# Kernel optimization log

Hardware: AMD Instinct MI355X
Metric: run time of the kernel (lower is better)

Reference implementation:

```python
import jax, jax.numpy as jnp
import numpy as np

S = 7  # output_size
B, C, HF, WF = 8, 256, 160, 160
N = 128
IMG = 640


def setup_inputs() -> dict:
    key = jax.random.key(0)
    k1, k2, k3, k4 = jax.random.split(key, 4)
    feature_map = jax.random.normal(k1, (B, C, HF, WF), jnp.float32)
    # boxes in image-pixel coordinates (the module divides by image_size itself)
    pts = jax.random.uniform(k2, (B, N, 2, 2), jnp.float32, 0.0, float(IMG))
    lo = jnp.min(pts, axis=2)  # (x1, y1)
    hi = jnp.max(pts, axis=2)  # (x2, y2)
    bboxes = jnp.concatenate([lo, hi], axis=-1)  # [B, N, 4]
    proj_w = jax.random.normal(k3, (C, C), jnp.float32) * (1.0 / np.sqrt(C))
    proj_b = jax.random.normal(k4, (C,), jnp.float32) * 0.01
    return {"feature_map": feature_map, "bboxes": bboxes,
            "proj_w": proj_w, "proj_b": proj_b,
            "image_h": IMG, "image_w": IMG}


def _forward(feature_map, bboxes, proj_w, proj_b, image_h, image_w):
    Bb, Cc, Hf, Wf = feature_map.shape
    # 1x1 conv projection
    f = jnp.einsum('bchw,oc->bohw', feature_map, proj_w) + proj_b[None, :, None, None]
    # scale boxes from image coords to feature coords, then integer clip (as in torch code)
    sx = float(Wf) / float(image_w)
    sy = float(Hf) / float(image_h)
    x1 = jnp.clip(jnp.floor(bboxes[..., 0] * sx).astype(jnp.int32), 0, Wf - 1)
    y1 = jnp.clip(jnp.floor(bboxes[..., 1] * sy).astype(jnp.int32), 0, Hf - 1)
    x2 = jnp.clip(jnp.floor(bboxes[..., 2] * sx).astype(jnp.int32), x1 + 1, Wf)
    y2 = jnp.clip(jnp.floor(bboxes[..., 3] * sy).astype(jnp.int32), y1 + 1, Hf)
    Lx = x2 - x1  # [B, N], >= 1 by construction
    Ly = y2 - y1
    i = jnp.arange(S, dtype=jnp.int32)
    # adaptive_avg_pool2d bin edges: start=floor(i*L/S), end=ceil((i+1)*L/S)
    rs = y1[..., None] + (i * Ly[..., None]) // S            # [B, N, S]
    re = y1[..., None] + ((i + 1) * Ly[..., None] + S - 1) // S
    cs = x1[..., None] + (i * Lx[..., None]) // S
    ce = x1[..., None] + ((i + 1) * Lx[..., None] + S - 1) // S
    # summed-area table (zero-padded): I[b,c,y,x] = sum of f[b,c,:y,:x]
    I = jnp.cumsum(jnp.cumsum(f, axis=2), axis=3)
    I = jnp.pad(I, ((0, 0), (0, 0), (1, 0), (1, 0)))

    def per_batch(Ib, rs_b, re_b, cs_b, ce_b):
        # Ib: [C, Hf+1, Wf+1]; index arrays: [N, S]
        tl = Ib[:, rs_b[:, :, None], cs_b[:, None, :]]
        tr = Ib[:, rs_b[:, :, None], ce_b[:, None, :]]
        bl = Ib[:, re_b[:, :, None], cs_b[:, None, :]]
        br = Ib[:, re_b[:, :, None], ce_b[:, None, :]]
        return br - tr - bl + tl  # [C, N, S, S]

    sums = jax.vmap(per_batch)(I, rs, re, cs, ce)  # [B, C, N, S, S]
    counts = ((re - rs)[..., :, None] * (ce - cs)[..., None, :]).astype(f.dtype)  # [B, N, S, S]
    region_features = jnp.transpose(sums, (0, 2, 1, 3, 4)) / counts[:, :, None, :, :]
    # area in raw bbox units, as in the original code
    area_ratios = (bboxes[..., 2] - bboxes[..., 0]) * (bboxes[..., 3] - bboxes[..., 1])
    return region_features, area_ratios


def reference(feature_map, bboxes, proj_w, proj_b, image_h, image_w):
    return _forward(feature_map, bboxes, proj_w, proj_b, image_h, image_w)
```

## Files before the change

### kernel.cpp

```cpp
#include <hip/hip_runtime.h>
#include <hip/hip_bf16.h>

#define BB 8
#define NN 128
#define CC 256
#define HFD 160
#define WFD 160
#define SS 7
#define REGION_OUT_ELEMS (8*128*256*49)

typedef short short8 __attribute__((ext_vector_type(8)));
typedef float f32x4  __attribute__((ext_vector_type(4)));

__global__ __launch_bounds__(256) void k0_convert_w(const float* __restrict__ W,
                                                    __hip_bfloat16* __restrict__ Wb) {
    int o = blockIdx.x;
    int c = threadIdx.x;
    Wb[o * CC + c] = __float2bfloat16(W[o * CC + c]);
}

__global__ __launch_bounds__(256) void k1_rowsum_transpose(const float* __restrict__ fm,
                                                           float* __restrict__ R) {
    int bid = blockIdx.x;
    int cq  = bid & 3;
    int bh  = bid >> 2;
    int h   = bh % HFD;
    int b   = bh / HFD;
    int c0  = cq * 64;
    int t   = threadIdx.x;

    __shared__ float tile[64][161];
    __shared__ float segsum[64][5];

    #pragma unroll
    for (int it = 0; it < 10; ++it) {
        int vid = it * 256 + t;
        int c_l = vid / 40;
        int wq  = vid - c_l * 40;
        float4 v = *(const float4*)(fm + (((size_t)(b * CC + c0 + c_l)) * HFD + h) * WFD + wq * 4);
        tile[c_l][wq * 4 + 0] = v.x;
        tile[c_l][wq * 4 + 1] = v.y;
        tile[c_l][wq * 4 + 2] = v.z;
        tile[c_l][wq * 4 + 3] = v.w;
    }
    __syncthreads();

    int seg = t >> 6;
    int row = t & 63;
    {
        float s = 0.f;
        int w0 = seg * 40;
        #pragma unroll 8
        for (int k = 0; k < 40; ++k) {
            s += tile[row][w0 + k];
            tile[row][w0 + k] = s;
        }
        segsum[row][seg] = s;
    }
    __syncthreads();
    if (t < 64) {
        float a0 = segsum[t][0];
        float a1 = a0 + segsum[t][1];
        float a2 = a1 + segsum[t][2];
        segsum[t][1] = a0;
        segsum[t][2] = a1;
        segsum[t][3] = a2;
    }
    __syncthreads();
    if (seg > 0) {
        float off = segsum[row][seg];
        int w0 = seg * 40;
        #pragma unroll 8
        for (int k = 0; k < 40; ++k) tile[row][w0 + k] += off;
    }
    __syncthreads();

    size_t obase = (((size_t)b * HFD + h) * WFD) * CC + c0;
    #pragma unroll
    for (int it = 0; it < 10; ++it) {
        int vid = it * 256 + t;
        int w   = vid >> 4;
        int cg  = vid & 15;
        float4 o;
        o.x = tile[cg * 4 + 0][w];
        o.y = tile[cg * 4 + 1][w];
        o.z = tile[cg * 4 + 2][w];
        o.w = tile[cg * 4 + 3][w];
        *(float4*)(R + obase + (size_t)w * CC + cg * 4) = o;
    }
}

__global__ __launch_bounds__(64) void k2_colsum(float* __restrict__ I) {
    int w = blockIdx.x % WFD;
    int b = blockIdx.x / WFD;
    int c4 = threadIdx.x * 4;
    float* p = I + (((size_t)b * HFD) * WFD + w) * CC + c4;
    const size_t stride = (size_t)WFD * CC;
    float sx = 0.f, sy = 0.f, sz = 0.f, sw = 0.f;
    #pragma unroll 8
    for (int h = 0; h < HFD; ++h) {
        float4 v = *(float4*)(p + (size_t)h * stride);
        sx += v.x; sy += v.y; sz += v.z; sw += v.w;
        float4 s = {sx, sy, sz, sw};
        *(float4*)(p + (size_t)h * stride) = s;
    }
}

#define PB_STRIDE 264

__global__ __launch_bounds__(256) void k3_gather_gemm(
        const float* __restrict__ I, const __hip_bfloat16* __restrict__ Wb,
        const float* __restrict__ bias, const float* __restrict__ bboxes,
        const int* __restrict__ ih_p, const int* __restrict__ iw_p,
        float* __restrict__ out) {
    int bn = blockIdx.x;
    int b  = bn >> 7;
    int t  = threadIdx.x;

    __shared__ __hip_bfloat16 Pb[64 * PB_STRIDE];

    float bx1 = bboxes[bn * 4 + 0];
    float by1 = bboxes[bn * 4 + 1];
    float bx2 = bboxes[bn * 4 + 2];
    float by2 = bboxes[bn * 4 + 3];
    float sx = (float)WFD / (float)iw_p[0];
    float sy = (float)HFD / (float)ih_p[0];

    int x1 = min(max((int)floorf(bx1 * sx), 0), WFD - 1);
    int y1 = min(max((int)floorf(by1 * sy), 0), HFD - 1);
    int x2 = min(max((int)floorf(bx2 * sx), x1 + 1), WFD);
    int y2 = min(max((int)floorf(by2 * sy), y1 + 1), HFD);
    int Lx = x2 - x1, Ly = y2 - y1;

    int rs[SS], re[SS], cs[SS], ce[SS];
    #pragma unroll
    for (int i = 0; i < SS; ++i) {
        rs[i] = y1 + (i * Ly) / SS;
        re[i] = y1 + ((i + 1) * Ly + SS - 1) / SS;
        cs[i] = x1 + (i * Lx) / SS;
        ce[i] = x1 + ((i + 1) * Lx + SS - 1) / SS;
    }

    #pragma unroll
    for (int r = 49; r < 64; ++r) Pb[r * PB_STRIDE + t] = __float2bfloat16(0.f);

    {
        const int c = t;
        const size_t Ib = (size_t)b * HFD * WFD * CC;
        #pragma unroll
        for (int i = 0; i < SS; ++i) {
            int r0 = rs[i] - 1, r1 = re[i] - 1;
            float rh = (float)(re[i] - rs[i]);
            #pragma unroll
            for (int j = 0; j < SS; ++j) {
                int c0 = cs[j] - 1, c1 = ce[j] - 1;
                float br = I[Ib + ((size_t)(r1 * WFD + c1)) * CC + c];
                float tr = (r0 >= 0) ? I[Ib + ((size_t)(r0 * WFD + c1)) * CC + c] : 0.f;
                float bl = (c0 >= 0) ? I[Ib + ((size_t)(r1 * WFD + c0)) * CC + c] : 0.f;
                float tl = (r0 >= 0 && c0 >= 0) ? I[Ib + ((size_t)(r0 * WFD + c0)) * CC + c] : 0.f;
                float cnt = rh * (float)(ce[j] - cs[j]);
                Pb[(i * SS + j) * PB_STRIDE + c] = __float2bfloat16((br - tr - bl + tl) / cnt);
            }
        }
    }
    __syncthreads();

    {
        const int lane = t & 63;
        const int wv   = t >> 6;
        const int ln   = lane & 15;
        const int quad = lane >> 4;
        const int ob0  = wv * 64;

        f32x4 z = {0.f, 0.f, 0.f, 0.f};
        f32x4 acc[4][4];
        #pragma unroll
        for (int mt = 0; mt < 4; ++mt)
            #pragma unroll
            for (int nt = 0; nt < 4; ++nt) acc[mt][nt] = z;

        #pragma unroll
        for (int k0 = 0; k0 < CC; k0 += 32) {
            short8 a[4], bf[4];
            #pragma unroll
            for (int mt = 0; mt < 4; ++mt)
                a[mt] = *(const short8*)((const short*)Wb + (ob0 + mt * 16 + ln) * CC + k0 + quad * 8);
            #pragma unroll
            for (int nt = 0; nt < 4; ++nt)
                bf[nt] = *(const short8*)((const short*)Pb + (nt * 16 + ln) * PB_STRIDE + k0 + quad * 8);
            #pragma unroll
            for (int mt = 0; mt < 4; ++mt)
                #pragma unroll
                for (int nt = 0; nt < 4; ++nt)
                    acc[mt][nt] = __builtin_amdgcn_mfma_f32_16x16x32_bf16(a[mt], bf[nt], acc[mt][nt], 0, 0, 0);
        }

        size_t obase = (size_t)bn * CC * 49;
        #pragma unroll
        for (int mt = 0; mt < 4; ++mt) {
            f32x4 bv = *(const f32x4*)(bias + ob0 + mt * 16 + quad * 4);
            #pragma unroll
            for (int nt = 0; nt < 4; ++nt) {
                int cell = nt * 16 + ln;
                if (cell < 49) {
                    #pragma unroll
                    for (int reg = 0; reg < 4; ++reg) {
                        int o = ob0 + mt * 16 + quad * 4 + reg;
                        out[obase + (size_t)o * 49 + cell] = acc[mt][nt][reg] + bv[reg];
                    }
                }
            }
        }
    }

    if (t == 0) {
        out[REGION_OUT_ELEMS + bn] = (bx2 - bx1) * (by2 - by1);
    }
}

extern "C" void kernel_launch(void* const* d_in, const int* in_sizes, int n_in,
                              void* d_out, int out_size, void* d_ws, size_t ws_size,
                              hipStream_t stream) {
    const float* fm     = (const float*)d_in[0];
    const float* bboxes = (const float*)d_in[1];
    const float* W      = (const float*)d_in[2];
    const float* bias   = (const float*)d_in[3];
    const int*   ih     = (const int*)d_in[4];
    const int*   iw     = (const int*)d_in[5];
    float* out = (float*)d_out;

    __hip_bfloat16* Wb = (__hip_bfloat16*)d_ws;
    float* I = (float*)((char*)d_ws + (size_t)CC * CC * 2 + 256);
    I = (float*)(((uintptr_t)I + 1023) & ~(uintptr_t)1023);

    k0_convert_w<<<CC, 256, 0, stream>>>(W, Wb);
    k1_rowsum_transpose<<<BB * HFD * 4, 256, 0, stream>>>(fm, I);
    k2_colsum<<<BB * WFD, 64, 0, stream>>>(I);
    k3_gather_gemm<<<BB * NN, 256, 0, stream>>>(I, Wb, bias, bboxes, ih, iw, out);
}
```

Baseline: 462.0 us.

## Split gather and GEMM into separate kernels, reorder SAT column/row scans

Moves the column prefix-sum onto the original NCHW feature map as its own kernel before the row-scan/transpose. Also splits the fused gather+GEMM into a gather kernel that writes pooled bf16 cells to a workspace and a GEMM kernel that packs 64 dense cells per block, so the 15 of 64 padding columns per box are no longer wasted. This costs an extra full-size fp32 intermediate buffer (C1) and an extra round trip of pooled data through global memory.

```diff
diff --git a/kernel.cpp b/kernel.cpp
--- a/kernel.cpp
+++ b/kernel.cpp
@@ -8,6 +8,7 @@
 #define WFD 160
 #define SS 7
 #define REGION_OUT_ELEMS (8*128*256*49)
+#define NTOT (BB*NN*49)
 
 typedef short short8 __attribute__((ext_vector_type(8)));
 typedef float f32x4  __attribute__((ext_vector_type(4)));
@@ -19,8 +20,22 @@
     Wb[o * CC + c] = __float2bfloat16(W[o * CC + c]);
 }
 
-__global__ __launch_bounds__(256) void k1_rowsum_transpose(const float* __restrict__ fm,
-                                                           float* __restrict__ R) {
+__global__ __launch_bounds__(256) void k1_colsum(const float* __restrict__ fm,
+                                                 float* __restrict__ C1) {
+    int g  = blockIdx.x * 256 + threadIdx.x;
+    int bc = g / WFD;
+    int w  = g - bc * WFD;
+    size_t base = (size_t)bc * (HFD * WFD) + w;
+    float s = 0.f;
+    #pragma unroll 8
+    for (int h = 0; h < HFD; ++h) {
+        s += fm[base + (size_t)h * WFD];
+        C1[base + (size_t)h * WFD] = s;
+    }
+}
+
+__global__ __launch_bounds__(256) void k2_rowsum_transpose(const float* __restrict__ C1,
+                                                           float* __restrict__ I) {
     int bid = blockIdx.x;
     int cq  = bid & 3;
     int bh  = bid >> 2;
@@ -37,7 +52,7 @@
         int vid = it * 256 + t;
         int c_l = vid / 40;
         int wq  = vid - c_l * 40;
-        float4 v = *(const float4*)(fm + (((size_t)(b * CC + c0 + c_l)) * HFD + h) * WFD + wq * 4);
+        float4 v = *(const float4*)(C1 + (((size_t)(b * CC + c0 + c_l)) * HFD + h) * WFD + wq * 4);
         tile[c_l][wq * 4 + 0] = v.x;
         tile[c_l][wq * 4 + 1] = v.y;
         tile[c_l][wq * 4 + 2] = v.z;
@@ -86,38 +101,17 @@
         o.y = tile[cg * 4 + 1][w];
         o.z = tile[cg * 4 + 2][w];
         o.w = tile[cg * 4 + 3][w];
-        *(float4*)(R + obase + (size_t)w * CC + cg * 4) = o;
-    }
-}
-
-__global__ __launch_bounds__(64) void k2_colsum(float* __restrict__ I) {
-    int w = blockIdx.x % WFD;
-    int b = blockIdx.x / WFD;
-    int c4 = threadIdx.x * 4;
-    float* p = I + (((size_t)b * HFD) * WFD + w) * CC + c4;
-    const size_t stride = (size_t)WFD * CC;
-    float sx = 0.f, sy = 0.f, sz = 0.f, sw = 0.f;
-    #pragma unroll 8
-    for (int h = 0; h < HFD; ++h) {
-        float4 v = *(float4*)(p + (size_t)h * stride);
-        sx += v.x; sy += v.y; sz += v.z; sw += v.w;
-        float4 s = {sx, sy, sz, sw};
-        *(float4*)(p + (size_t)h * stride) = s;
-    }
-}
-
-#define PB_STRIDE 264
-
-__global__ __launch_bounds__(256) void k3_gather_gemm(
-        const float* __restrict__ I, const __hip_bfloat16* __restrict__ Wb,
-        const float* __restrict__ bias, const float* __restrict__ bboxes,
+        *(float4*)(I + obase + (size_t)w * CC + cg * 4) = o;
+    }
+}
+
+__global__ __launch_bounds__(256) void k3_gather(
+        const float* __restrict__ I, const float* __restrict__ bboxes,
         const int* __restrict__ ih_p, const int* __restrict__ iw_p,
-        float* __restrict__ out) {
+        __hip_bfloat16* __restrict__ P, float* __restrict__ out) {
     int bn = blockIdx.x;
     int b  = bn >> 7;
     int t  = threadIdx.x;
-
-    __shared__ __hip_bfloat16 Pb[64 * PB_STRIDE];
 
     float bx1 = bboxes[bn * 4 + 0];
     float by1 = bboxes[bn * 4 + 1];
@@ -141,80 +135,93 @@
         ce[i] = x1 + ((i + 1) * Lx + SS - 1) / SS;
     }
 
-    #pragma unroll
-    for (int r = 49; r < 64; ++r) Pb[r * PB_STRIDE + t] = __float2bfloat16(0.f);
-
-    {
-        const int c = t;
-        const size_t Ib = (size_t)b * HFD * WFD * CC;
-        #pragma unroll
-        for (int i = 0; i < SS; ++i) {
-            int r0 = rs[i] - 1, r1 = re[i] - 1;
-            float rh = (float)(re[i] - rs[i]);
+    const int c = t;
+    const size_t Ib = (size_t)b * HFD * WFD * CC;
+    size_t pbase = (size_t)bn * 49 * CC + c;
+    #pragma unroll
+    for (int i = 0; i < SS; ++i) {
+        int r0 = rs[i] - 1, r1 = re[i] - 1;
+        float rh = (float)(re[i] - rs[i]);
+        #pragma unroll
+        for (int j = 0; j < SS; ++j) {
+            int c0 = cs[j] - 1, c1 = ce[j] - 1;
+            float br = I[Ib + ((size_t)(r1 * WFD + c1)) * CC + c];
+            float tr = (r0 >= 0) ? I[Ib + ((size_t)(r0 * WFD + c1)) * CC + c] : 0.f;
+            float bl = (c0 >= 0) ? I[Ib + ((size_t)(r1 * WFD + c0)) * CC + c] : 0.f;
+            float tl = (r0 >= 0 && c0 >= 0) ? I[Ib + ((size_t)(r0 * WFD + c0)) * CC + c] : 0.f;
+            float cnt = rh * (float)(ce[j] - cs[j]);
+            P[pbase + (size_t)(i * SS + j) * CC] = __float2bfloat16((br - tr - bl + tl) / cnt);
+        }
+    }
+
+    if (t == 0) {
+        out[REGION_OUT_ELEMS + bn] = (bx2 - bx1) * (by2 - by1);
+    }
+}
+
+#define PB_STRIDE 264
+
+__global__ __launch_bounds__(256) void k4_gemm(
+        const __hip_bfloat16* __restrict__ P, const __hip_bfloat16* __restrict__ Wb,
+        const float* __restrict__ bias, float* __restrict__ out) {
+    int n0 = blockIdx.x * 64;
+    int t  = threadIdx.x;
+
+    __shared__ __hip_bfloat16 Pb[64 * PB_STRIDE];
+
+    #pragma unroll
+    for (int it = 0; it < 8; ++it) {
+        int vid = it * 256 + t;
+        int row = vid >> 5;
+        int cq  = vid & 31;
+        short8 v = *(const short8*)((const short*)P + ((size_t)(n0 + row)) * CC + cq * 8);
+        *(short8*)((short*)Pb + row * PB_STRIDE + cq * 8) = v;
+    }
+    __syncthreads();
+
+    const int lane = t & 63;
+    const int wv   = t >> 6;
+    const int ln   = lane & 15;
+    const int quad = lane >> 4;
+    const int ob0  = wv * 64;
+
+    f32x4 z = {0.f, 0.f, 0.f, 0.f};
+    f32x4 acc[4][4];
+    #pragma unroll
+    for (int mt = 0; mt < 4; ++mt)
+        #pragma unroll
+        for (int nt = 0; nt < 4; ++nt) acc[mt][nt] = z;
+
+    #pragma unroll
+    for (int k0 = 0; k0 < CC; k0 += 32) {
+        short8 a[4], bf[4];
+        #pragma unroll
+        for (int mt = 0; mt < 4; ++mt)
+            a[mt] = *(const short8*)((const short*)Wb + (ob0 + mt * 16 + ln) * CC + k0 + quad * 8);
+        #pragma unroll
+        for (int nt = 0; nt < 4; ++nt)
+            bf[nt] = *(const short8*)((const short*)Pb + (nt * 16 + ln) * PB_STRIDE + k0 + quad * 8);
+        #pragma unroll
+        for (int mt = 0; mt < 4; ++mt)
             #pragma unroll
-            for (int j = 0; j < SS; ++j) {
-                int c0 = cs[j] - 1, c1 = ce[j] - 1;
-                float br = I[Ib + ((size_t)(r1 * WFD + c1)) * CC + c];
-                float tr = (r0 >= 0) ? I[Ib + ((size_t)(r0 * WFD + c1)) * CC + c] : 0.f;
-                float bl = (c0 >= 0) ? I[Ib + ((size_t)(r1 * WFD + c0)) * CC + c] : 0.f;
-                float tl = (r0 >= 0 && c0 >= 0) ? I[Ib + ((size_t)(r0 * WFD + c0)) * CC + c] : 0.f;
-                float cnt = rh * (float)(ce[j] - cs[j]);
-                Pb[(i * SS + j) * PB_STRIDE + c] = __float2bfloat16((br - tr - bl + tl) / cnt);
+            for (int nt = 0; nt < 4; ++nt)
+                acc[mt][nt] = __builtin_amdgcn_mfma_f32_16x16x32_bf16(a[mt], bf[nt], acc[mt][nt], 0, 0, 0);
+    }
+
+    #pragma unroll
+    for (int mt = 0; mt < 4; ++mt) {
+        f32x4 bv = *(const f32x4*)(bias + ob0 + mt * 16 + quad * 4);
+        #pragma unroll
+        for (int nt = 0; nt < 4; ++nt) {
+            int cellg = n0 + nt * 16 + ln;
+            int bn    = cellg / 49;
+            int cell  = cellg - bn * 49;
+            size_t base = (size_t)bn * (CC * 49) + (size_t)(ob0 + mt * 16 + quad * 4) * 49 + cell;
+            #pragma unroll
+            for (int reg = 0; reg < 4; ++reg) {
+                out[base + (size_t)reg * 49] = acc[mt][nt][reg] + bv[reg];
             }
         }
-    }
-    __syncthreads();
-
-    {
-        const int lane = t & 63;
-        const int wv   = t >> 6;
-        const int ln   = lane & 15;
-        const int quad = lane >> 4;
-        const int ob0  = wv * 64;
-
-        f32x4 z = {0.f, 0.f, 0.f, 0.f};
-        f32x4 acc[4][4];
-        #pragma unroll
-        for (int mt = 0; mt < 4; ++mt)
-            #pragma unroll
-            for (int nt = 0; nt < 4; ++nt) acc[mt][nt] = z;
-
-        #pragma unroll
-        for (int k0 = 0; k0 < CC; k0 += 32) {
-            short8 a[4], bf[4];
-            #pragma unroll
-            for (int mt = 0; mt < 4; ++mt)
-                a[mt] = *(const short8*)((const short*)Wb + (ob0 + mt * 16 + ln) * CC + k0 + quad * 8);
-            #pragma unroll
-            for (int nt = 0; nt < 4; ++nt)
-                bf[nt] = *(const short8*)((const short*)Pb + (nt * 16 + ln) * PB_STRIDE + k0 + quad * 8);
-            #pragma unroll
-            for (int mt = 0; mt < 4; ++mt)
-                #pragma unroll
-                for (int nt = 0; nt < 4; ++nt)
-                    acc[mt][nt] = __builtin_amdgcn_mfma_f32_16x16x32_bf16(a[mt], bf[nt], acc[mt][nt], 0, 0, 0);
-        }
-
-        size_t obase = (size_t)bn * CC * 49;
-        #pragma unroll
-        for (int mt = 0; mt < 4; ++mt) {
-            f32x4 bv = *(const f32x4*)(bias + ob0 + mt * 16 + quad * 4);
-            #pragma unroll
-            for (int nt = 0; nt < 4; ++nt) {
-                int cell = nt * 16 + ln;
-                if (cell < 49) {
-                    #pragma unroll
-                    for (int reg = 0; reg < 4; ++reg) {
-                        int o = ob0 + mt * 16 + quad * 4 + reg;
-                        out[obase + (size_t)o * 49 + cell] = acc[mt][nt][reg] + bv[reg];
-                    }
-                }
-            }
-        }
-    }
-
-    if (t == 0) {
-        out[REGION_OUT_ELEMS + bn] = (bx2 - bx1) * (by2 - by1);
     }
 }
 
@@ -229,12 +236,16 @@
     const int*   iw     = (const int*)d_in[5];
     float* out = (float*)d_out;
 
-    __hip_bfloat16* Wb = (__hip_bfloat16*)d_ws;
-    float* I = (float*)((char*)d_ws + (size_t)CC * CC * 2 + 256);
-    I = (float*)(((uintptr_t)I + 1023) & ~(uintptr_t)1023);
-
-    k0_convert_w<<<CC, 256, 0, stream>>>(W, Wb);
-    k1_rowsum_transpose<<<BB * HFD * 4, 256, 0, stream>>>(fm, I);
-    k2_colsum<<<BB * WFD, 64, 0, stream>>>(I);
-    k3_gather_gemm<<<BB * NN, 256, 0, stream>>>(I, Wb, bias, bboxes, ih, iw, out);
-}
+    const size_t FM_BYTES = (size_t)BB * CC * HFD * WFD * 4;
+    char* ws = (char*)d_ws;
+    __hip_bfloat16* Wb = (__hip_bfloat16*)ws;
+    float* C1 = (float*)(ws + 131072);
+    float* I  = (float*)(ws + 131072 + FM_BYTES);
+    __hip_bfloat16* P = (__hip_bfloat16*)(ws + 131072 + 2 * FM_BYTES);
+
+    k0_convert_w       <<<CC, 256, 0, stream>>>(W, Wb);
+    k1_colsum          <<<(BB * CC * WFD) / 256, 256, 0, stream>>>(fm, C1);
+    k2_rowsum_transpose<<<BB * HFD * 4, 256, 0, stream>>>(C1, I);
+    k3_gather          <<<BB * NN, 256, 0, stream>>>(I, bboxes, ih, iw, P, out);
+    k4_gemm            <<<NTOT / 64, 256, 0, stream>>>(P, Wb, bias, out);
+}
```

Result: slower. 513.2 us (+11.1%).
